# Kernel optimization log

Hardware: AMD Instinct MI355X
Metric: run time of the kernel (lower is better)

Reference implementation:

```python
import jax, jax.numpy as jnp
import numpy as np

E = 8        # n_routed_experts
Z = 4        # zero_expert_num (identity experts)
K = 2        # moe_topk
SCALE = 2.5  # routed_scaling_factor
T, H, I = 8192, 1024, 512


def setup_inputs() -> dict:
    key = jax.random.key(0)
    k0, k1, k2, k3, k4 = jax.random.split(key, 5)
    return {
        "hidden_states": jax.random.normal(k0, (T, H), jnp.float32),
        "router_w": jax.random.normal(k1, (E + Z, H), jnp.float32) * 0.02,
        "correction_bias": jax.random.normal(k2, (E + Z,), jnp.float32) * 0.01,
        "w13": jax.random.normal(k3, (E, 2 * I, H), jnp.float32) * 0.02,
        "w2": jax.random.normal(k4, (E, H, I), jnp.float32) * 0.02,
    }


def reference(hidden_states, router_w, correction_bias, w13, w2):
    # ---- router (float32) ----
    logits = hidden_states.astype(jnp.float32) @ router_w.T          # [T, E+Z]
    scores = jax.nn.softmax(logits, axis=-1)
    # correction bias only affects expert *selection*, not the gate weights
    _, topk_idx = jax.lax.top_k(scores + correction_bias, K)          # [T, K]
    topk_w = jnp.take_along_axis(scores, topk_idx, axis=-1)          # renormalize=False

    # ---- zero experts (identity type): idx >= E contributes scale * x ----
    is_zero = topk_idx >= E                                           # [T, K]
    routed_w = jnp.where(is_zero, 0.0, topk_w)
    zero_scale = jnp.where(is_zero, topk_w, 0.0).sum(-1, keepdims=True)
    zero_result = zero_scale * hidden_states                          # [T, H]

    # ---- combine weights per routed expert: [T, E] ----
    tok = jnp.arange(hidden_states.shape[0])[:, None]
    safe_idx = jnp.clip(topk_idx, 0, E - 1)   # zero-expert slots carry weight 0
    combine = jnp.zeros((hidden_states.shape[0], E), scores.dtype)
    combine = combine.at[tok, safe_idx].add(routed_w)

    # ---- grouped expert GEMMs (SiLU gated MLP), combined densely ----
    h = jnp.einsum('th,eih->eti', hidden_states, w13)                 # [E, T, 2I]
    g, u = jnp.split(h, 2, axis=-1)
    act = jax.nn.silu(g) * u                                          # [E, T, I]
    eo = jnp.einsum('eti,ehi->eth', act, w2)                          # [E, T, H]
    routed = jnp.einsum('te,eth->th', combine, eo)                    # [T, H]

    return routed * SCALE + zero_result
```

## Files before the change

kernel.cpp:

```cpp
#include <hip/hip_runtime.h>
#include <hip/hip_bf16.h>
#include <math.h>

typedef __bf16 bf16_t;
typedef bf16_t bf16x4 __attribute__((ext_vector_type(4)));
typedef bf16_t bf16x8 __attribute__((ext_vector_type(8)));
typedef float f32x4 __attribute__((ext_vector_type(4)));

#define T_TOK 8192
#define HDIM  1024
#define IDIM  512
#define NEXP  8
#define NTOT  12
#define MAXROWS (2 * T_TOK + NEXP * 128)
#define MAX_MTILES (MAXROWS / 128)
#define WCAST_BLOCKS 6144
#define R_BLOCKS 512

__device__ __forceinline__ void gll16(const bf16_t* g, bf16_t* l) {
  __builtin_amdgcn_global_load_lds((__attribute__((address_space(1))) void*)g,
                                   (__attribute__((address_space(3))) void*)l,
                                   16, 0, 0);
}

__global__ __launch_bounds__(256) void wcast_kernel(
    const float* __restrict__ w13, const float* __restrict__ w2,
    bf16_t* __restrict__ w13b, bf16_t* __restrict__ w2b,
    int* __restrict__ sel_tok, float* __restrict__ sel_w) {
  size_t gid = (size_t)blockIdx.x * blockDim.x + threadIdx.x;
  if (gid < MAXROWS) { sel_tok[gid] = 0; sel_w[gid] = 0.f; }
  const size_t n13 = (size_t)NEXP * 2 * IDIM * HDIM / 8;
  const float* in; bf16_t* outp; size_t i;
  if (gid < n13) { in = w13; outp = w13b; i = gid * 8; }
  else           { in = w2;  outp = w2b;  i = (gid - n13) * 8; }
  float4 a = *(const float4*)&in[i];
  float4 b = *(const float4*)&in[i + 4];
  bf16x8 o;
  o[0] = (bf16_t)a.x; o[1] = (bf16_t)a.y; o[2] = (bf16_t)a.z; o[3] = (bf16_t)a.w;
  o[4] = (bf16_t)b.x; o[5] = (bf16_t)b.y; o[6] = (bf16_t)b.z; o[7] = (bf16_t)b.w;
  *(bf16x8*)&outp[i] = o;
}

__global__ __launch_bounds__(256) void router_kernel(
    const float* __restrict__ x, const float* __restrict__ rw,
    const float* __restrict__ bias,
    bf16_t* __restrict__ xb,
    int* __restrict__ tk_e, float* __restrict__ tk_w, float* __restrict__ zscale) {
  __shared__ float rws[NTOT * HDIM];
  const int bid = blockIdx.x;
  const int tid = threadIdx.x;
#pragma unroll
  for (int i = 0; i < NTOT * HDIM / 4 / 256; i++)
    ((float4*)rws)[i * 256 + tid] = ((const float4*)rw)[i * 256 + tid];
  __syncthreads();
  const int wv = tid >> 6, l = tid & 63;
  const int tbase = bid * 16 + wv * 4;
  for (int k = 0; k < 4; k++) {
    int t = tbase + k;
    const float4* xr = (const float4*)(x + (size_t)t * HDIM);
    float4 xv[4];
#pragma unroll
    for (int i = 0; i < 4; i++) xv[i] = xr[l + 64 * i];
#pragma unroll
    for (int i = 0; i < 4; i++) {
      bf16x4 o;
      o[0] = (bf16_t)xv[i].x; o[1] = (bf16_t)xv[i].y;
      o[2] = (bf16_t)xv[i].z; o[3] = (bf16_t)xv[i].w;
      *(bf16x4*)&xb[(size_t)t * HDIM + (size_t)(l + 64 * i) * 4] = o;
    }
    float part[NTOT];
#pragma unroll
    for (int e = 0; e < NTOT; e++) {
      const float4* wr = (const float4*)(rws + e * HDIM);
      float s = 0.f;
#pragma unroll
      for (int i = 0; i < 4; i++) {
        float4 w = wr[l + 64 * i];
        s += xv[i].x * w.x + xv[i].y * w.y + xv[i].z * w.z + xv[i].w * w.w;
      }
      part[e] = s;
    }
#pragma unroll
    for (int off = 32; off > 0; off >>= 1)
#pragma unroll
      for (int e = 0; e < NTOT; e++) part[e] += __shfl_down(part[e], off);

    if (l == 0) {
      float mx = part[0];
#pragma unroll
      for (int e = 1; e < NTOT; e++) mx = fmaxf(mx, part[e]);
      float p[NTOT], den = 0.f;
#pragma unroll
      for (int e = 0; e < NTOT; e++) { p[e] = expf(part[e] - mx); den += p[e]; }
      float inv = 1.f / den;
#pragma unroll
      for (int e = 0; e < NTOT; e++) p[e] *= inv;
      float s0 = -1e30f, s1 = -1e30f; int i0 = 0, i1 = 0;
#pragma unroll
      for (int e = 0; e < NTOT; e++) {
        float v = p[e] + bias[e];
        if (v > s0) { s1 = s0; i1 = i0; s0 = v; i0 = e; }
        else if (v > s1) { s1 = v; i1 = e; }
      }
      float zs = 0.f;
      int idx[2] = { i0, i1 };
#pragma unroll
      for (int kk = 0; kk < 2; kk++) {
        int e = idx[kk];
        float w = p[e];
        if (e >= NEXP) { zs += w; tk_e[2 * t + kk] = -1; tk_w[2 * t + kk] = 0.f; }
        else           { tk_e[2 * t + kk] = e; tk_w[2 * t + kk] = w; }
      }
      zscale[t] = zs;
    }
  }
}

__global__ void countscan_kernel(const int* __restrict__ tk_e, int* __restrict__ cursor,
                                 int* __restrict__ total_rows, int* __restrict__ tile_e,
                                 int* __restrict__ tile_p0, int* __restrict__ n_mtiles) {
  __shared__ int lc[NEXP];
  int tid = threadIdx.x;
  if (tid < NEXP) lc[tid] = 0;
  __syncthreads();
  int cnt[NEXP];
#pragma unroll
  for (int j = 0; j < NEXP; j++) cnt[j] = 0;
  for (int i = tid; i < 2 * T_TOK; i += 256) {
    int e = tk_e[i];
#pragma unroll
    for (int j = 0; j < NEXP; j++) cnt[j] += (e == j) ? 1 : 0;
  }
#pragma unroll
  for (int off = 32; off > 0; off >>= 1)
#pragma unroll
    for (int j = 0; j < NEXP; j++) cnt[j] += __shfl_down(cnt[j], off);
  if ((tid & 63) == 0)
#pragma unroll
    for (int j = 0; j < NEXP; j++) atomicAdd(&lc[j], cnt[j]);
  __syncthreads();
  if (tid == 0) {
    int run = 0, nt = 0;
    for (int e = 0; e < NEXP; e++) {
      cursor[e] = run;
      int ntile = (lc[e] + 127) / 128;
      for (int i = 0; i < ntile; i++) {
        tile_e[nt] = e;
        tile_p0[nt] = run + i * 128;
        nt++;
      }
      run += ntile * 128;
    }
    *total_rows = run;
    *n_mtiles = nt;
  }
}

__global__ void assign_kernel(const int* __restrict__ tk_e, const float* __restrict__ tk_w,
                              int* __restrict__ cursor, int* __restrict__ sel_tok,
                              float* __restrict__ sel_w, int* __restrict__ pos) {
  __shared__ int lc[NEXP];
  __shared__ int lbase[NEXP];
  int tid = threadIdx.x;
  if (tid < NEXP) lc[tid] = 0;
  __syncthreads();
  int t = blockIdx.x * blockDim.x + tid;
  int e0 = tk_e[2 * t], e1 = tk_e[2 * t + 1];
  int r0 = (e0 >= 0) ? atomicAdd(&lc[e0], 1) : -1;
  int r1 = (e1 >= 0) ? atomicAdd(&lc[e1], 1) : -1;
  __syncthreads();
  if (tid < NEXP) lbase[tid] = atomicAdd(&cursor[tid], lc[tid]);
  __syncthreads();
  int p0 = -1, p1 = -1;
  if (e0 >= 0) { p0 = lbase[e0] + r0; sel_tok[p0] = t; sel_w[p0] = 2.5f * tk_w[2 * t]; }
  if (e1 >= 0) { p1 = lbase[e1] + r1; sel_tok[p1] = t; sel_w[p1] = 2.5f * tk_w[2 * t + 1]; }
  pos[2 * t] = p0;
  pos[2 * t + 1] = p1;
}

__global__ __launch_bounds__(256, 2) void gemm1_kernel(
    const bf16_t* __restrict__ xb, const bf16_t* __restrict__ w13b,
    const int* __restrict__ sel_tok, const int* __restrict__ tile_e,
    const int* __restrict__ tile_p0, const int* __restrict__ n_mtiles,
    bf16_t* __restrict__ actb) {
  const int b = blockIdx.x;
  const int xk = b & 7, j = b >> 3;
  const int ti = xk + 8 * (j >> 2);
  const int g0 = (j & 3) * 128;
  if (ti >= *n_mtiles) return;
  const int e = tile_e[ti];
  const int p0 = tile_p0[ti];

  __shared__ alignas(16) bf16_t As[128 * 64];
  __shared__ alignas(16) bf16_t Bs[256 * 64];
  const int tid = threadIdx.x;
  const int w = tid >> 6, l = tid & 63;
  const int wr = w >> 1, wc = w & 1;
  const int quad = l >> 4, c16 = l & 15;

  const int srow = tid >> 3;
  const int csrc = ((tid & 7) ^ (srow & 7)) * 8;
  const bf16_t* w13e = w13b + (size_t)e * (2 * IDIM) * HDIM;
  const bf16_t* Asrc[4];
  const bf16_t* Bsrc[8];
#pragma unroll
  for (int s = 0; s < 4; s++) {
    int tok = sel_tok[p0 + s * 32 + srow];
    Asrc[s] = xb + (size_t)tok * HDIM + csrc;
  }
#pragma unroll
  for (int s = 0; s < 8; s++) {
    int col = g0 + (s >> 1) * 32 + srow + ((s & 1) ? IDIM : 0);
    Bsrc[s] = w13e + (size_t)col * HDIM + csrc;
  }

  f32x4 acc[4][8];
#pragma unroll
  for (int i = 0; i < 4; i++)
#pragma unroll
    for (int j2 = 0; j2 < 8; j2++) acc[i][j2] = (f32x4){0.f, 0.f, 0.f, 0.f};

  for (int k0 = 0; k0 < HDIM; k0 += 64) {
#pragma unroll
    for (int s = 0; s < 4; s++) gll16(Asrc[s] + k0, &As[s * 2048 + w * 512]);
#pragma unroll
    for (int s = 0; s < 8; s++) gll16(Bsrc[s] + k0, &Bs[s * 2048 + w * 512]);
    __syncthreads();
#pragma unroll
    for (int kk = 0; kk < 2; kk++) {
      const int kch = ((kk * 4 + quad) ^ (c16 & 7)) * 8;
      bf16x8 af[4], bfv[8];
#pragma unroll
      for (int mt = 0; mt < 4; mt++)
        af[mt] = *(const bf16x8*)&As[(wr * 64 + mt * 16 + c16) * 64 + kch];
#pragma unroll
      for (int nt = 0; nt < 8; nt++)
        bfv[nt] = *(const bf16x8*)&Bs[(wc * 128 + nt * 16 + c16) * 64 + kch];
#pragma unroll
      for (int mt = 0; mt < 4; mt++)
#pragma unroll
        for (int nt = 0; nt < 8; nt++)
          acc[mt][nt] = __builtin_amdgcn_mfma_f32_16x16x32_bf16(af[mt], bfv[nt], acc[mt][nt], 0, 0, 0);
    }
    __syncthreads();
  }

#pragma unroll
  for (int mt = 0; mt < 4; mt++) {
    int rowb = p0 + wr * 64 + mt * 16 + quad * 4;
#pragma unroll
    for (int ntg = 0; ntg < 4; ntg++) {
      int nt = (ntg & 1) + (ntg >> 1) * 4;
      int col = g0 + (wc * 2 + (nt >> 2)) * 32 + (nt & 1) * 16 + c16;
#pragma unroll
      for (int r = 0; r < 4; r++) {
        float g = acc[mt][nt][r];
        float u = acc[mt][nt + 2][r];
        float s = g / (1.f + expf(-g));
        actb[(size_t)(rowb + r) * IDIM + col] = (bf16_t)(s * u);
      }
    }
  }
}

__global__ __launch_bounds__(256, 2) void gemm2_kernel(
    const bf16_t* __restrict__ actb, const bf16_t* __restrict__ w2b,
    const float* __restrict__ sel_w, const int* __restrict__ tile_e,
    const int* __restrict__ tile_p0, const int* __restrict__ n_mtiles,
    bf16_t* __restrict__ eob) {
  const int b = blockIdx.x;
  const int xk = b & 7, j = b >> 3;
  const int ti = xk + 8 * (j >> 2);
  const int n0 = (j & 3) * 256;
  if (ti >= *n_mtiles) return;
  const int e = tile_e[ti];
  const int p0 = tile_p0[ti];

  __shared__ alignas(16) bf16_t As[128 * 64];
  __shared__ alignas(16) bf16_t Bs[256 * 64];
  const int tid = threadIdx.x;
  const int w = tid >> 6, l = tid & 63;
  const int wr = w >> 1, wc = w & 1;
  const int quad = l >> 4, c16 = l & 15;

  const int srow = tid >> 3;
  const int csrc = ((tid & 7) ^ (srow & 7)) * 8;
  const bf16_t* w2e = w2b + (size_t)e * HDIM * IDIM;
  const bf16_t* Asrc[4];
  const bf16_t* Bsrc[8];
#pragma unroll
  for (int s = 0; s < 4; s++)
    Asrc[s] = actb + (size_t)(p0 + s * 32 + srow) * IDIM + csrc;
#pragma unroll
  for (int s = 0; s < 8; s++)
    Bsrc[s] = w2e + (size_t)(n0 + s * 32 + srow) * IDIM + csrc;

  f32x4 acc[4][8];
#pragma unroll
  for (int i = 0; i < 4; i++)
#pragma unroll
    for (int j2 = 0; j2 < 8; j2++) acc[i][j2] = (f32x4){0.f, 0.f, 0.f, 0.f};

  for (int k0 = 0; k0 < IDIM; k0 += 64) {
#pragma unroll
    for (int s = 0; s < 4; s++) gll16(Asrc[s] + k0, &As[s * 2048 + w * 512]);
#pragma unroll
    for (int s = 0; s < 8; s++) gll16(Bsrc[s] + k0, &Bs[s * 2048 + w * 512]);
    __syncthreads();
#pragma unroll
    for (int kk = 0; kk < 2; kk++) {
      const int kch = ((kk * 4 + quad) ^ (c16 & 7)) * 8;
      bf16x8 af[4], bfv[8];
#pragma unroll
      for (int mt = 0; mt < 4; mt++)
        af[mt] = *(const bf16x8*)&As[(wr * 64 + mt * 16 + c16) * 64 + kch];
#pragma unroll
      for (int nt = 0; nt < 8; nt++)
        bfv[nt] = *(const bf16x8*)&Bs[(wc * 128 + nt * 16 + c16) * 64 + kch];
#pragma unroll
      for (int mt = 0; mt < 4; mt++)
#pragma unroll
        for (int nt = 0; nt < 8; nt++)
          acc[mt][nt] = __builtin_amdgcn_mfma_f32_16x16x32_bf16(af[mt], bfv[nt], acc[mt][nt], 0, 0, 0);
    }
    __syncthreads();
  }

#pragma unroll
  for (int mt = 0; mt < 4; mt++) {
    int rowb = wr * 64 + mt * 16 + quad * 4;
    float cw[4];
#pragma unroll
    for (int r = 0; r < 4; r++) cw[r] = sel_w[p0 + rowb + r];
#pragma unroll
    for (int nt = 0; nt < 8; nt++) {
      int col = n0 + wc * 128 + nt * 16 + c16;
#pragma unroll
      for (int r = 0; r < 4; r++)
        eob[(size_t)(p0 + rowb + r) * HDIM + col] = (bf16_t)(cw[r] * acc[mt][nt][r]);
    }
  }
}

__global__ void combine_kernel(const float* __restrict__ x, const float* __restrict__ zscale,
                               const int* __restrict__ pos, const bf16_t* __restrict__ eob,
                               float* __restrict__ out) {
  size_t gid = (size_t)blockIdx.x * blockDim.x + threadIdx.x;
  size_t t = gid >> 7;
  size_t j = (gid & 127) << 3;
  float zs = zscale[t];
  int p0 = pos[2 * t], p1 = pos[2 * t + 1];
  float4 a = *(const float4*)&x[t * HDIM + j];
  float4 b = *(const float4*)&x[t * HDIM + j + 4];
  float o[8] = { zs * a.x, zs * a.y, zs * a.z, zs * a.w,
                 zs * b.x, zs * b.y, zs * b.z, zs * b.w };
  if (p0 >= 0) {
    bf16x8 v = *(const bf16x8*)&eob[(size_t)p0 * HDIM + j];
#pragma unroll
    for (int k = 0; k < 8; k++) o[k] += (float)v[k];
  }
  if (p1 >= 0) {
    bf16x8 v = *(const bf16x8*)&eob[(size_t)p1 * HDIM + j];
#pragma unroll
    for (int k = 0; k < 8; k++) o[k] += (float)v[k];
  }
  *(float4*)&out[t * HDIM + j] = make_float4(o[0], o[1], o[2], o[3]);
  *(float4*)&out[t * HDIM + j + 4] = make_float4(o[4], o[5], o[6], o[7]);
}

extern "C" void kernel_launch(void* const* d_in, const int* in_sizes, int n_in,
                              void* d_out, int out_size, void* d_ws, size_t ws_size,
                              hipStream_t stream) {
  const float* x    = (const float*)d_in[0];
  const float* rw   = (const float*)d_in[1];
  const float* bias = (const float*)d_in[2];
  const float* w13  = (const float*)d_in[3];
  const float* w2   = (const float*)d_in[4];
  float* out = (float*)d_out;

  char* ws = (char*)d_ws;
  bf16_t* w13b = (bf16_t*)ws;  ws += (size_t)NEXP * 2 * IDIM * HDIM * 2;
  bf16_t* w2b  = (bf16_t*)ws;  ws += (size_t)NEXP * HDIM * IDIM * 2;
  bf16_t* xb   = (bf16_t*)ws;  ws += (size_t)T_TOK * HDIM * 2;
  bf16_t* actb = (bf16_t*)ws;  ws += (size_t)MAXROWS * IDIM * 2;
  bf16_t* eob  = (bf16_t*)ws;  ws += (size_t)MAXROWS * HDIM * 2;
  int*   tk_e    = (int*)ws;   ws += (size_t)T_TOK * 2 * 4;
  float* tk_w    = (float*)ws; ws += (size_t)T_TOK * 2 * 4;
  float* zscale  = (float*)ws; ws += (size_t)T_TOK * 4;
  int*   pos     = (int*)ws;   ws += (size_t)T_TOK * 2 * 4;
  int*   sel_tok = (int*)ws;   ws += (size_t)MAXROWS * 4;
  float* sel_w   = (float*)ws; ws += (size_t)MAXROWS * 4;
  int*   cursor  = (int*)ws;   ws += NEXP * 4;
  int*   total_rows = (int*)ws; ws += 4;
  int*   tile_e  = (int*)ws;   ws += MAX_MTILES * 4;
  int*   tile_p0 = (int*)ws;   ws += MAX_MTILES * 4;
  int*   n_mtiles = (int*)ws;  ws += 4;

  wcast_kernel<<<WCAST_BLOCKS, 256, 0, stream>>>(w13, w2, w13b, w2b, sel_tok, sel_w);
  router_kernel<<<R_BLOCKS, 256, 0, stream>>>(x, rw, bias, xb, tk_e, tk_w, zscale);
  countscan_kernel<<<1, 256, 0, stream>>>(tk_e, cursor, total_rows,
                                          tile_e, tile_p0, n_mtiles);
  assign_kernel<<<T_TOK / 256, 256, 0, stream>>>(tk_e, tk_w, cursor, sel_tok, sel_w, pos);

  gemm1_kernel<<<MAX_MTILES * ((2 * IDIM) / 256), 256, 0, stream>>>(
      xb, w13b, sel_tok, tile_e, tile_p0, n_mtiles, actb);
  gemm2_kernel<<<MAX_MTILES * (HDIM / 256), 256, 0, stream>>>(
      actb, w2b, sel_w, tile_e, tile_p0, n_mtiles, eob);

  combine_kernel<<<(size_t)T_TOK * HDIM / 8 / 256, 256, 0, stream>>>(
      x, zscale, pos, eob, out);
}
```

Baseline: 231.4 us.

## Double-buffer LDS tiles with K=32 steps in both expert GEMM kernels

Both grouped GEMM kernels drop the single-buffered BK=64 LDS tile and use two BK=32 buffers instead. The next tile's global_load_lds is issued before the MFMAs on the current tile, so global-memory latency overlaps with compute and each iteration needs one barrier instead of two. The LDS swizzle and per-thread load mapping change to fit the narrower 32-element rows. Total LDS stays the same, but there are twice as many loop iterations, each with fewer MFMAs per barrier.

```diff
diff --git a/kernel.cpp b/kernel.cpp
--- a/kernel.cpp
+++ b/kernel.cpp
@@ -191,26 +191,26 @@
   const int e = tile_e[ti];
   const int p0 = tile_p0[ti];
 
-  __shared__ alignas(16) bf16_t As[128 * 64];
-  __shared__ alignas(16) bf16_t Bs[256 * 64];
+  __shared__ alignas(16) bf16_t As[2 * 128 * 32];
+  __shared__ alignas(16) bf16_t Bs[2 * 256 * 32];
   const int tid = threadIdx.x;
   const int w = tid >> 6, l = tid & 63;
   const int wr = w >> 1, wc = w & 1;
   const int quad = l >> 4, c16 = l & 15;
 
-  const int srow = tid >> 3;
-  const int csrc = ((tid & 7) ^ (srow & 7)) * 8;
+  const int rr = tid >> 2;
+  const int csrc = ((tid & 3) ^ ((rr >> 1) & 3)) * 8;
   const bf16_t* w13e = w13b + (size_t)e * (2 * IDIM) * HDIM;
-  const bf16_t* Asrc[4];
-  const bf16_t* Bsrc[8];
+  const bf16_t* Asrc[2];
+  const bf16_t* Bsrc[4];
+#pragma unroll
+  for (int s = 0; s < 2; s++) {
+    int tok = sel_tok[p0 + s * 64 + rr];
+    Asrc[s] = xb + (size_t)tok * HDIM + csrc;
+  }
 #pragma unroll
   for (int s = 0; s < 4; s++) {
-    int tok = sel_tok[p0 + s * 32 + srow];
-    Asrc[s] = xb + (size_t)tok * HDIM + csrc;
-  }
-#pragma unroll
-  for (int s = 0; s < 8; s++) {
-    int col = g0 + (s >> 1) * 32 + srow + ((s & 1) ? IDIM : 0);
+    int col = g0 + s * 32 + (rr & 31) + (((rr >> 5) & 1) ? IDIM : 0);
     Bsrc[s] = w13e + (size_t)col * HDIM + csrc;
   }
 
@@ -220,29 +220,36 @@
 #pragma unroll
     for (int j2 = 0; j2 < 8; j2++) acc[i][j2] = (f32x4){0.f, 0.f, 0.f, 0.f};
 
-  for (int k0 = 0; k0 < HDIM; k0 += 64) {
-#pragma unroll
-    for (int s = 0; s < 4; s++) gll16(Asrc[s] + k0, &As[s * 2048 + w * 512]);
-#pragma unroll
-    for (int s = 0; s < 8; s++) gll16(Bsrc[s] + k0, &Bs[s * 2048 + w * 512]);
+#pragma unroll
+  for (int s = 0; s < 2; s++) gll16(Asrc[s], &As[s * 2048 + w * 512]);
+#pragma unroll
+  for (int s = 0; s < 4; s++) gll16(Bsrc[s], &Bs[s * 2048 + w * 512]);
+  __syncthreads();
+
+  const int kch = (quad ^ ((c16 >> 1) & 3)) * 8;
+  int cur = 0;
+  for (int t = 0; t < HDIM / 32; ++t) {
+    if (t + 1 < HDIM / 32) {
+      const int k0 = (t + 1) * 32, nb = cur ^ 1;
+#pragma unroll
+      for (int s = 0; s < 2; s++) gll16(Asrc[s] + k0, &As[nb * 4096 + s * 2048 + w * 512]);
+#pragma unroll
+      for (int s = 0; s < 4; s++) gll16(Bsrc[s] + k0, &Bs[nb * 8192 + s * 2048 + w * 512]);
+    }
+    bf16x8 af[4], bfv[8];
+#pragma unroll
+    for (int mt = 0; mt < 4; mt++)
+      af[mt] = *(const bf16x8*)&As[cur * 4096 + (wr * 64 + mt * 16 + c16) * 32 + kch];
+#pragma unroll
+    for (int nt = 0; nt < 8; nt++)
+      bfv[nt] = *(const bf16x8*)&Bs[cur * 8192 + (wc * 128 + nt * 16 + c16) * 32 + kch];
+#pragma unroll
+    for (int mt = 0; mt < 4; mt++)
+#pragma unroll
+      for (int nt = 0; nt < 8; nt++)
+        acc[mt][nt] = __builtin_amdgcn_mfma_f32_16x16x32_bf16(af[mt], bfv[nt], acc[mt][nt], 0, 0, 0);
     __syncthreads();
-#pragma unroll
-    for (int kk = 0; kk < 2; kk++) {
-      const int kch = ((kk * 4 + quad) ^ (c16 & 7)) * 8;
-      bf16x8 af[4], bfv[8];
-#pragma unroll
-      for (int mt = 0; mt < 4; mt++)
-        af[mt] = *(const bf16x8*)&As[(wr * 64 + mt * 16 + c16) * 64 + kch];
-#pragma unroll
-      for (int nt = 0; nt < 8; nt++)
-        bfv[nt] = *(const bf16x8*)&Bs[(wc * 128 + nt * 16 + c16) * 64 + kch];
-#pragma unroll
-      for (int mt = 0; mt < 4; mt++)
-#pragma unroll
-        for (int nt = 0; nt < 8; nt++)
-          acc[mt][nt] = __builtin_amdgcn_mfma_f32_16x16x32_bf16(af[mt], bfv[nt], acc[mt][nt], 0, 0, 0);
-    }
-    __syncthreads();
+    cur ^= 1;
   }
 
 #pragma unroll
@@ -276,24 +283,24 @@
   const int e = tile_e[ti];
   const int p0 = tile_p0[ti];
 
-  __shared__ alignas(16) bf16_t As[128 * 64];
-  __shared__ alignas(16) bf16_t Bs[256 * 64];
+  __shared__ alignas(16) bf16_t As[2 * 128 * 32];
+  __shared__ alignas(16) bf16_t Bs[2 * 256 * 32];
   const int tid = threadIdx.x;
   const int w = tid >> 6, l = tid & 63;
   const int wr = w >> 1, wc = w & 1;
   const int quad = l >> 4, c16 = l & 15;
 
-  const int srow = tid >> 3;
-  const int csrc = ((tid & 7) ^ (srow & 7)) * 8;
+  const int rr = tid >> 2;
+  const int csrc = ((tid & 3) ^ ((rr >> 1) & 3)) * 8;
   const bf16_t* w2e = w2b + (size_t)e * HDIM * IDIM;
-  const bf16_t* Asrc[4];
-  const bf16_t* Bsrc[8];
+  const bf16_t* Asrc[2];
+  const bf16_t* Bsrc[4];
+#pragma unroll
+  for (int s = 0; s < 2; s++)
+    Asrc[s] = actb + (size_t)(p0 + s * 64 + rr) * IDIM + csrc;
 #pragma unroll
   for (int s = 0; s < 4; s++)
-    Asrc[s] = actb + (size_t)(p0 + s * 32 + srow) * IDIM + csrc;
-#pragma unroll
-  for (int s = 0; s < 8; s++)
-    Bsrc[s] = w2e + (size_t)(n0 + s * 32 + srow) * IDIM + csrc;
+    Bsrc[s] = w2e + (size_t)(n0 + s * 64 + rr) * IDIM + csrc;
 
   f32x4 acc[4][8];
 #pragma unroll
@@ -301,29 +308,36 @@
 #pragma unroll
     for (int j2 = 0; j2 < 8; j2++) acc[i][j2] = (f32x4){0.f, 0.f, 0.f, 0.f};
 
-  for (int k0 = 0; k0 < IDIM; k0 += 64) {
-#pragma unroll
-    for (int s = 0; s < 4; s++) gll16(Asrc[s] + k0, &As[s * 2048 + w * 512]);
-#pragma unroll
-    for (int s = 0; s < 8; s++) gll16(Bsrc[s] + k0, &Bs[s * 2048 + w * 512]);
+#pragma unroll
+  for (int s = 0; s < 2; s++) gll16(Asrc[s], &As[s * 2048 + w * 512]);
+#pragma unroll
+  for (int s = 0; s < 4; s++) gll16(Bsrc[s], &Bs[s * 2048 + w * 512]);
+  __syncthreads();
+
+  const int kch = (quad ^ ((c16 >> 1) & 3)) * 8;
+  int cur = 0;
+  for (int t = 0; t < IDIM / 32; ++t) {
+    if (t + 1 < IDIM / 32) {
+      const int k0 = (t + 1) * 32, nb = cur ^ 1;
+#pragma unroll
+      for (int s = 0; s < 2; s++) gll16(Asrc[s] + k0, &As[nb * 4096 + s * 2048 + w * 512]);
+#pragma unroll
+      for (int s = 0; s < 4; s++) gll16(Bsrc[s] + k0, &Bs[nb * 8192 + s * 2048 + w * 512]);
+    }
+    bf16x8 af[4], bfv[8];
+#pragma unroll
+    for (int mt = 0; mt < 4; mt++)
+      af[mt] = *(const bf16x8*)&As[cur * 4096 + (wr * 64 + mt * 16 + c16) * 32 + kch];
+#pragma unroll
+    for (int nt = 0; nt < 8; nt++)
+      bfv[nt] = *(const bf16x8*)&Bs[cur * 8192 + (wc * 128 + nt * 16 + c16) * 32 + kch];
+#pragma unroll
+    for (int mt = 0; mt < 4; mt++)
+#pragma unroll
+      for (int nt = 0; nt < 8; nt++)
+        acc[mt][nt] = __builtin_amdgcn_mfma_f32_16x16x32_bf16(af[mt], bfv[nt], acc[mt][nt], 0, 0, 0);
     __syncthreads();
-#pragma unroll
-    for (int kk = 0; kk < 2; kk++) {
-      const int kch = ((kk * 4 + quad) ^ (c16 & 7)) * 8;
-      bf16x8 af[4], bfv[8];
-#pragma unroll
-      for (int mt = 0; mt < 4; mt++)
-        af[mt] = *(const bf16x8*)&As[(wr * 64 + mt * 16 + c16) * 64 + kch];
-#pragma unroll
-      for (int nt = 0; nt < 8; nt++)
-        bfv[nt] = *(const bf16x8*)&Bs[(wc * 128 + nt * 16 + c16) * 64 + kch];
-#pragma unroll
-      for (int mt = 0; mt < 4; mt++)
-#pragma unroll
-        for (int nt = 0; nt < 8; nt++)
-          acc[mt][nt] = __builtin_amdgcn_mfma_f32_16x16x32_bf16(af[mt], bfv[nt], acc[mt][nt], 0, 0, 0);
-    }
-    __syncthreads();
+    cur ^= 1;
   }
 
 #pragma unroll
```

Result: slower. 246.4 us (+6.5%).
